# Kernel tuning notes

Measured on AMD Instinct MI355X. Metric: run time of the kernel, lower is better.

## Reference

```python
import jax, jax.numpy as jnp
import numpy as np

B, S, D, H = 4, 2048, 1024, 16
HD = D // H  # head_dim = 64


def setup_inputs() -> dict:
    key = jax.random.key(0)
    ks = jax.random.split(key, 12)
    scale = 1.0 / np.sqrt(D)
    inp = {
        "q": jax.random.normal(ks[0], (B, S, D), jnp.float32),
        "k": jax.random.normal(ks[1], (B, S, D), jnp.float32),
        "v": jax.random.normal(ks[2], (B, S, D), jnp.float32),
        # additive-style mask: 1 = blocked (causal upper triangle)
        "mask": jnp.triu(jnp.ones((S, S), jnp.float32), k=1)[None, None, :, :],
        "Wq": jax.random.normal(ks[3], (D, D), jnp.float32) * scale,
        "bq": jnp.zeros((D,), jnp.float32),
        "Wk": jax.random.normal(ks[4], (D, D), jnp.float32) * scale,
        "bk": jnp.zeros((D,), jnp.float32),
        "Wv": jax.random.normal(ks[5], (D, D), jnp.float32) * scale,
        "bv": jnp.zeros((D,), jnp.float32),
        "Wo": jax.random.normal(ks[6], (D, D), jnp.float32) * scale,
        "bo": jnp.zeros((D,), jnp.float32),
    }
    return inp


def _split_heads(x):
    # [B, S, D] -> [B, H, S, HD]
    b, s, _ = x.shape
    return x.reshape(b, s, H, HD).transpose(0, 2, 1, 3)


def reference(q, k, v, mask, Wq, bq, Wk, bk, Wv, bv, Wo, bo):
    qh = _split_heads(q @ Wq.T + bq)
    kh = _split_heads(k @ Wk.T + bk)
    vh = _split_heads(v @ Wv.T + bv)
    # full [B, H, S, S] score matrix (faithful to the naive implementation)
    logits = jnp.einsum("bhqd,bhkd->bhqk", qh, kh) / jnp.sqrt(jnp.float32(HD))
    logits = logits + mask * -1e9
    weights = jax.nn.softmax(logits, axis=-1)
    attn = jnp.einsum("bhqk,bhkd->bhqd", weights, vh)  # [B, H, S, HD]
    attn = attn.transpose(0, 2, 1, 3).reshape(q.shape[0], -1, D)
    return attn @ Wo.T + bo
```

## Files before the change

### kernel.cpp

```cpp
#include <hip/hip_runtime.h>
#include <stdint.h>

typedef __attribute__((ext_vector_type(8))) short short8;
typedef __attribute__((ext_vector_type(4))) float f32x4;
typedef __attribute__((ext_vector_type(4))) unsigned short ushort4v;
typedef __attribute__((ext_vector_type(8))) unsigned short ushort8v;

#define MFMA(a, b, c) __builtin_amdgcn_mfma_f32_16x16x32_bf16((a), (b), (c), 0, 0, 0)

__device__ __forceinline__ unsigned short f2bf(float f) {
  union { float f; unsigned u; } x; x.f = f;
  return (unsigned short)((x.u + 0x7FFFu + ((x.u >> 16) & 1u)) >> 16);
}

__device__ __forceinline__ unsigned short f2bf_trunc(float f) {
  union { float f; unsigned u; } x; x.f = f;
  return (unsigned short)(x.u >> 16);
}

#define GLL(gp, lp)                                                             \
  __builtin_amdgcn_global_load_lds(                                             \
      (const __attribute__((address_space(1))) unsigned int*)(const void*)(gp), \
      (__attribute__((address_space(3))) unsigned int*)(lp), 16, 0, 0)

__global__ void cvt6_bf16(const float* __restrict__ s0, const float* __restrict__ s1,
                          const float* __restrict__ s2, const float* __restrict__ s3,
                          const float* __restrict__ s4, const float* __restrict__ s5,
                          unsigned short* __restrict__ d0, unsigned short* __restrict__ d1,
                          unsigned short* __restrict__ d2, unsigned short* __restrict__ d3,
                          unsigned short* __restrict__ d4, unsigned short* __restrict__ d5,
                          int nBig, int nSmall) {
  const int y = blockIdx.y;
  const float* s = y == 0 ? s0 : (y == 1 ? s1 : (y == 2 ? s2 :
                   (y == 3 ? s3 : (y == 4 ? s4 : s5))));
  unsigned short* d = y == 0 ? d0 : (y == 1 ? d1 : (y == 2 ? d2 :
                      (y == 3 ? d3 : (y == 4 ? d4 : d5))));
  const int n8 = (y < 3) ? nBig : nSmall;
  int i = blockIdx.x * blockDim.x + threadIdx.x;
  int stride = gridDim.x * blockDim.x;
  for (; i < n8; i += stride) {
    float4 a = ((const float4*)s)[2 * i];
    float4 b = ((const float4*)s)[2 * i + 1];
    ushort8v o;
    o[0] = f2bf(a.x); o[1] = f2bf(a.y); o[2] = f2bf(a.z); o[3] = f2bf(a.w);
    o[4] = f2bf(b.x); o[5] = f2bf(b.y); o[6] = f2bf(b.z); o[7] = f2bf(b.w);
    ((ushort8v*)d)[i] = o;
  }
}

__global__ void cvt_bf16(const float* __restrict__ s, unsigned short* __restrict__ d,
                         int n4) {
  int i = blockIdx.x * blockDim.x + threadIdx.x;
  int stride = gridDim.x * blockDim.x;
  for (; i < n4; i += stride) {
    float4 v = ((const float4*)s)[i];
    ushort4v o;
    o[0] = f2bf(v.x); o[1] = f2bf(v.y); o[2] = f2bf(v.z); o[3] = f2bf(v.w);
    ((ushort4v*)d)[i] = o;
  }
}

template <int OUT_MODE>
__global__ __launch_bounds__(256, 2) void gemm64(
    const unsigned short* __restrict__ A, const unsigned short* __restrict__ W,
    const float* __restrict__ bias, void* __restrict__ Out, float oscale) {
  const int K = 1024, N = 1024;
  __shared__ unsigned short As[2][8192];
  __shared__ unsigned short Bs[2][8192];
  const int tid = threadIdx.x;
  const int lane = tid & 63;
  const int wid = tid >> 6;
  const int l15 = lane & 15, l4 = lane >> 4;
  const int bm = blockIdx.y * 128, bn = blockIdx.x * 128;
  const int wm = (wid >> 1) * 64, wn = (wid & 1) * 64;
  const int srl8 = lane >> 3;
  const int sc8 = ((lane & 7) ^ srl8) * 8;

  f32x4 acc[4][4] = {};

#define STAGE(buf, ktv)                                                        \
  {                                                                            \
    const int kb0 = (ktv) * 64;                                                \
    _Pragma("unroll") for (int i = 0; i < 4; ++i) {                            \
      GLL(&A[(size_t)(bm + i * 32 + wid * 8 + srl8) * K + kb0 + sc8],          \
          &As[buf][i * 2048 + wid * 512]);                                     \
      GLL(&W[(size_t)(bn + i * 32 + wid * 8 + srl8) * K + kb0 + sc8],          \
          &Bs[buf][i * 2048 + wid * 512]);                                     \
    }                                                                          \
  }

  STAGE(0, 0)
  __syncthreads();
  int cur = 0;
  const int NK = K / 64;
  for (int kt = 0; kt < NK; ++kt) {
    if (kt + 1 < NK) STAGE(cur ^ 1, kt + 1)
#pragma unroll
    for (int ks = 0; ks < 2; ++ks) {
      short8 af[4], bfr[4];
#pragma unroll
      for (int i = 0; i < 4; ++i) {
        const int ra = wm + i * 16 + l15;
        const int rb = wn + i * 16 + l15;
        af[i] = *(const short8*)(
            &As[cur][ra * 64 + (((ks * 4 + l4) ^ (ra & 7)) * 8)]);
        bfr[i] = *(const short8*)(
            &Bs[cur][rb * 64 + (((ks * 4 + l4) ^ (rb & 7)) * 8)]);
      }
#pragma unroll
      for (int mi = 0; mi < 4; ++mi)
#pragma unroll
        for (int ni = 0; ni < 4; ++ni)
          acc[mi][ni] = MFMA(af[mi], bfr[ni], acc[mi][ni]);
    }
    __syncthreads();
    cur ^= 1;
  }
#undef STAGE

  float bv[4];
#pragma unroll
  for (int ni = 0; ni < 4; ++ni) bv[ni] = bias[bn + wn + ni * 16 + l15];

#pragma unroll
  for (int mi = 0; mi < 4; ++mi) {
#pragma unroll
    for (int ni = 0; ni < 4; ++ni) {
      const int gn = bn + wn + ni * 16 + l15;
      if constexpr (OUT_MODE == 2) {
        float* Of = (float*)Out;
#pragma unroll
        for (int r = 0; r < 4; ++r) {
          int gm = bm + wm + mi * 16 + l4 * 4 + r;
          Of[(size_t)gm * N + gn] = acc[mi][ni][r] + bv[ni];
        }
      } else {
        unsigned short* Ob = (unsigned short*)Out;
        const int h = gn >> 6, hd = gn & 63;
#pragma unroll
        for (int r = 0; r < 4; ++r) {
          int gm = bm + wm + mi * 16 + l4 * 4 + r;
          int b = gm >> 11, s = gm & 2047;
          Ob[((size_t)(b * 16 + h) * 2048 + s) * 64 + hd] =
              f2bf((acc[mi][ni][r] + bv[ni]) * oscale);
        }
      }
    }
  }
}

__global__ __launch_bounds__(256, 2) void gemm64_kv(
    const unsigned short* __restrict__ A0, const unsigned short* __restrict__ W0,
    const float* __restrict__ bias0, unsigned short* __restrict__ Out0,
    const unsigned short* __restrict__ A1, const unsigned short* __restrict__ W1,
    const float* __restrict__ bias1, unsigned short* __restrict__ Out1) {
  const int K = 1024;
  __shared__ unsigned short As[2][8192];
  __shared__ unsigned short Bs[2][8192];
  const int tid = threadIdx.x;
  const int lane = tid & 63;
  const int wid = tid >> 6;
  const int l15 = lane & 15, l4 = lane >> 4;
  const int proj = blockIdx.y >> 6;
  const int bm = (blockIdx.y & 63) * 128, bn = blockIdx.x * 128;
  const int wm = (wid >> 1) * 64, wn = (wid & 1) * 64;
  const int srl8 = lane >> 3;
  const int sc8 = ((lane & 7) ^ srl8) * 8;

  const unsigned short* A = proj == 0 ? A0 : A1;
  const unsigned short* W = proj == 0 ? W0 : W1;
  const float* bias = proj == 0 ? bias0 : bias1;
  unsigned short* Out = proj == 0 ? Out0 : Out1;

  f32x4 acc[4][4] = {};

#define STAGE(buf, ktv)                                                        \
  {                                                                            \
    const int kb0 = (ktv) * 64;                                                \
    _Pragma("unroll") for (int i = 0; i < 4; ++i) {                            \
      GLL(&A[(size_t)(bm + i * 32 + wid * 8 + srl8) * K + kb0 + sc8],          \
          &As[buf][i * 2048 + wid * 512]);                                     \
      GLL(&W[(size_t)(bn + i * 32 + wid * 8 + srl8) * K + kb0 + sc8],          \
          &Bs[buf][i * 2048 + wid * 512]);                                     \
    }                                                                          \
  }

  STAGE(0, 0)
  __syncthreads();
  int cur = 0;
  const int NK = K / 64;
  for (int kt = 0; kt < NK; ++kt) {
    if (kt + 1 < NK) STAGE(cur ^ 1, kt + 1)
#pragma unroll
    for (int ks = 0; ks < 2; ++ks) {
      short8 af[4], bfr[4];
#pragma unroll
      for (int i = 0; i < 4; ++i) {
        const int ra = wm + i * 16 + l15;
        const int rb = wn + i * 16 + l15;
        af[i] = *(const short8*)(
            &As[cur][ra * 64 + (((ks * 4 + l4) ^ (ra & 7)) * 8)]);
        bfr[i] = *(const short8*)(
            &Bs[cur][rb * 64 + (((ks * 4 + l4) ^ (rb & 7)) * 8)]);
      }
#pragma unroll
      for (int mi = 0; mi < 4; ++mi)
#pragma unroll
        for (int ni = 0; ni < 4; ++ni)
          acc[mi][ni] = MFMA(af[mi], bfr[ni], acc[mi][ni]);
    }
    __syncthreads();
    cur ^= 1;
  }
#undef STAGE

  float bv[4];
#pragma unroll
  for (int ni = 0; ni < 4; ++ni) bv[ni] = bias[bn + wn + ni * 16 + l15];

#pragma unroll
  for (int mi = 0; mi < 4; ++mi) {
#pragma unroll
    for (int ni = 0; ni < 4; ++ni) {
      const int gn = bn + wn + ni * 16 + l15;
      const int h = gn >> 6, hd = gn & 63;
      if (proj == 0) {
#pragma unroll
        for (int r = 0; r < 4; ++r) {
          int gm = bm + wm + mi * 16 + l4 * 4 + r;
          int b = gm >> 11, s = gm & 2047;
          Out[((size_t)(b * 16 + h) * 2048 + s) * 64 + hd] =
              f2bf(acc[mi][ni][r] + bv[ni]);
        }
      } else {
        int gm0 = bm + wm + mi * 16 + l4 * 4;
        int b = gm0 >> 11, s0 = gm0 & 2047;
        ushort4v t;
#pragma unroll
        for (int r = 0; r < 4; ++r) t[r] = f2bf(acc[mi][ni][r] + bv[ni]);
        *(ushort4v*)(Out + ((size_t)(b * 16 + h) * 64 + hd) * 2048 + s0) = t;
      }
    }
  }
}

__global__ __launch_bounds__(256, 3) void attn_kernel(
    const unsigned short* __restrict__ qh, const unsigned short* __restrict__ kh,
    const unsigned short* __restrict__ vt, unsigned short* __restrict__ aout) {
  const int S = 2048, HD = 64;
  __shared__ unsigned short Kt[2][4096];
  __shared__ unsigned short Vt[2][4096];
  __shared__ unsigned short P_lds[4][32 * 72];
  const int tid = threadIdx.x;
  const int wid = tid >> 6, lane = tid & 63;
  const int l15 = lane & 15, l4 = lane >> 4;
  const int bh = blockIdx.x;
  const int b = bh >> 4, h = bh & 15;
  const int yb = 15 - (int)blockIdx.y;
  const int q0 = yb * 128 + wid * 32;
  const unsigned short* Qp = qh + (size_t)bh * S * HD;
  const unsigned short* Kp = kh + (size_t)bh * S * HD;
  const unsigned short* Vp = vt + (size_t)bh * HD * S;
  unsigned short* pl = P_lds[wid];

  const int srl = lane >> 3;
  const int swz = ((lane & 7) ^ srl) * 8;
  const int rb0 = wid * 16, rb1 = wid * 16 + 8;

  short8 vone;
#pragma unroll
  for (int j = 0; j < 8; ++j) vone[j] = (short)0x3F80;

  short8 qa[2][2];
#pragma unroll
  for (int mt = 0; mt < 2; ++mt)
#pragma unroll
    for (int hh = 0; hh < 2; ++hh)
      qa[mt][hh] = *(const short8*)(Qp + (size_t)(q0 + mt * 16 + l15) * HD +
                                    hh * 32 + l4 * 8);

  f32x4 Oacc[2][5] = {};

#define STAGEKV(buf, kbv)                                                      \
  {                                                                            \
    const int k0s = (kbv) << 6;                                                \
    GLL(Kp + (size_t)(k0s + rb0 + srl) * 64 + swz, &Kt[buf][rb0 * 64]);        \
    GLL(Kp + (size_t)(k0s + rb1 + srl) * 64 + swz, &Kt[buf][rb1 * 64]);        \
    GLL(Vp + (size_t)(rb0 + srl) * S + k0s + swz, &Vt[buf][rb0 * 64]);         \
    GLL(Vp + (size_t)(rb1 + srl) * S + k0s + swz, &Vt[buf][rb1 * 64]);         \
  }

  const int nkb = 2 * yb + 2;
  STAGEKV(0, 0)
  __syncthreads();
  int cur = 0;
  for (int kb = 0; kb < nkb; ++kb) {
    const int key0 = kb << 6;
    if (kb + 1 < nkb) STAGEKV(cur ^ 1, kb + 1)

    if (key0 <= q0 + 31) {
      const bool needmask = (key0 + 63 > q0);
      short8 kfr[4][2];
#pragma unroll
      for (int kf = 0; kf < 4; ++kf) {
        const int kr = kf * 16 + l15;
        kfr[kf][0] =
            *(const short8*)(&Kt[cur][kr * 64 + ((l4 ^ (l15 & 7)) * 8)]);
        kfr[kf][1] =
            *(const short8*)(&Kt[cur][kr * 64 + (((4 + l4) ^ (l15 & 7)) * 8)]);
      }
#pragma unroll
      for (int mt = 0; mt < 2; ++mt) {
#pragma unroll
        for (int kf = 0; kf < 4; ++kf) {
          f32x4 z = {};
          z = MFMA(kfr[kf][0], qa[mt][0], z);
          z = MFMA(kfr[kf][1], qa[mt][1], z);
          if (needmask) {
            int qrow = q0 + mt * 16 + l15;
#pragma unroll
            for (int r = 0; r < 4; ++r) {
              int key = key0 + kf * 16 + l4 * 4 + r;
              if (key > qrow) z[r] = -3.0e38f;
            }
          }
          unsigned short* pw = &pl[(mt * 16 + l15) * 72 + kf * 16 + l4 * 4];
#pragma unroll
          for (int r = 0; r < 4; ++r)
            pw[r] = f2bf_trunc(__builtin_amdgcn_exp2f(z[r]));
        }
      }
      short8 vb[4][2];
#pragma unroll
      for (int ni = 0; ni < 4; ++ni) {
        const int vr = ni * 16 + l15;
#pragma unroll
        for (int kc = 0; kc < 2; ++kc)
          vb[ni][kc] = *(const short8*)(
              &Vt[cur][vr * 64 + (((kc * 4 + l4) ^ (l15 & 7)) * 8)]);
      }
      short8 pa[2][2];
#pragma unroll
      for (int mt = 0; mt < 2; ++mt)
#pragma unroll
        for (int kc = 0; kc < 2; ++kc)
          pa[mt][kc] =
              *(const short8*)(&pl[(mt * 16 + l15) * 72 + kc * 32 + l4 * 8]);
#pragma unroll
      for (int mt = 0; mt < 2; ++mt) {
#pragma unroll
        for (int ni = 0; ni < 4; ++ni) {
          Oacc[mt][ni] = MFMA(pa[mt][0], vb[ni][0], Oacc[mt][ni]);
          Oacc[mt][ni] = MFMA(pa[mt][1], vb[ni][1], Oacc[mt][ni]);
        }
        Oacc[mt][4] = MFMA(pa[mt][0], vone, Oacc[mt][4]);
        Oacc[mt][4] = MFMA(pa[mt][1], vone, Oacc[mt][4]);
      }
    }
    __syncthreads();
    cur ^= 1;
  }
#undef STAGEKV

#pragma unroll
  for (int mt = 0; mt < 2; ++mt) {
    float inv[4];
#pragma unroll
    for (int r = 0; r < 4; ++r) inv[r] = __builtin_amdgcn_rcpf(Oacc[mt][4][r]);
#pragma unroll
    for (int ni = 0; ni < 4; ++ni)
#pragma unroll
      for (int r = 0; r < 4; ++r) {
        int row = q0 + mt * 16 + l4 * 4 + r;
        aout[((size_t)(b * 2048 + row)) * 1024 + h * 64 + ni * 16 + l15] =
            f2bf(Oacc[mt][ni][r] * inv[r]);
      }
  }
}

extern "C" void kernel_launch(void* const* d_in, const int* in_sizes, int n_in,
                              void* d_out, int out_size, void* d_ws,
                              size_t ws_size, hipStream_t stream) {
  const float* q = (const float*)d_in[0];
  const float* k = (const float*)d_in[1];
  const float* v = (const float*)d_in[2];
  const float* Wq = (const float*)d_in[4];
  const float* bq = (const float*)d_in[5];
  const float* Wk = (const float*)d_in[6];
  const float* bk = (const float*)d_in[7];
  const float* Wv = (const float*)d_in[8];
  const float* bv = (const float*)d_in[9];
  const float* Wo = (const float*)d_in[10];
  const float* bo = (const float*)d_in[11];

  const size_t MT = (size_t)8192 * 1024;
  unsigned short* qh    = (unsigned short*)d_ws;
  unsigned short* kh    = qh + MT;
  unsigned short* vt    = kh + MT;
  unsigned short* attnb = vt + MT;
  unsigned short* Ab  = (unsigned short*)d_out;
  unsigned short* Wqb = Ab + MT;
  unsigned short* Wkb = Wqb + 1024 * 1024;
  unsigned short* Wvb = Wkb + 1024 * 1024;
  unsigned short* Wob = qh;

  dim3 gg(8, 64), bb(256);
  const int nW4 = 1024 * 1024 / 4;
  const int nW8 = 1024 * 1024 / 8, nA8 = (int)(MT / 8);

  cvt6_bf16<<<dim3(1024, 6), bb, 0, stream>>>(q, k, v, Wq, Wk, Wv,
                                              kh, Ab, attnb, Wqb, Wkb, Wvb,
                                              nA8, nW8);
  gemm64<0><<<gg, bb, 0, stream>>>(kh, Wqb, bq, qh, 0.18033688011112042f);
  gemm64_kv<<<dim3(8, 128), bb, 0, stream>>>(Ab, Wkb, bk, kh, attnb, Wvb, bv, vt);

  attn_kernel<<<dim3(64, 16), bb, 0, stream>>>(qh, kh, vt, attnb);

  cvt_bf16<<<256, bb, 0, stream>>>(Wo, Wob, nW4);
  gemm64<2><<<gg, bb, 0, stream>>>(attnb, Wob, bo, (float*)d_out, 1.0f);
}
```

Measured before the change: 177.2 us.

## Split each attention block's key range across warp pairs and reduce partials in LDS

```diff
diff --git a/kernel.cpp b/kernel.cpp
--- a/kernel.cpp
+++ b/kernel.cpp
@@ -256,8 +256,9 @@
   const int l15 = lane & 15, l4 = lane >> 4;
   const int bh = blockIdx.x;
   const int b = bh >> 4, h = bh & 15;
-  const int yb = 15 - (int)blockIdx.y;
-  const int q0 = yb * 128 + wid * 32;
+  const int qb = 31 - (int)blockIdx.y;
+  const int g = wid >> 1, hf = wid & 1;
+  const int q0 = qb * 64 + g * 32;
   const unsigned short* Qp = qh + (size_t)bh * S * HD;
   const unsigned short* Kp = kh + (size_t)bh * S * HD;
   const unsigned short* Vp = vt + (size_t)bh * HD * S;
@@ -281,33 +282,38 @@
 
   f32x4 Oacc[2][5] = {};
 
-#define STAGEKV(buf, kbv)                                                      \
-  {                                                                            \
-    const int k0s = (kbv) << 6;                                                \
-    GLL(Kp + (size_t)(k0s + rb0 + srl) * 64 + swz, &Kt[buf][rb0 * 64]);        \
-    GLL(Kp + (size_t)(k0s + rb1 + srl) * 64 + swz, &Kt[buf][rb1 * 64]);        \
-    GLL(Vp + (size_t)(rb0 + srl) * S + k0s + swz, &Vt[buf][rb0 * 64]);         \
-    GLL(Vp + (size_t)(rb1 + srl) * S + k0s + swz, &Vt[buf][rb1 * 64]);         \
-  }
-
-  const int nkb = 2 * yb + 2;
-  STAGEKV(0, 0)
-  __syncthreads();
-  int cur = 0;
-  for (int kb = 0; kb < nkb; ++kb) {
-    const int key0 = kb << 6;
-    if (kb + 1 < nkb) STAGEKV(cur ^ 1, kb + 1)
-
-    if (key0 <= q0 + 31) {
-      const bool needmask = (key0 + 63 > q0);
+  const int nt = qb + 1;
+  const int NS = (qb >> 1) + 1;
+  for (int s = 0; s < NS; ++s) {
+    const int tA = 2 * s, tB = 2 * s + 1;
+    {
+      const int k0A = tA << 6;
+      GLL(Kp + (size_t)(k0A + rb0 + srl) * 64 + swz, &Kt[0][rb0 * 64]);
+      GLL(Kp + (size_t)(k0A + rb1 + srl) * 64 + swz, &Kt[0][rb1 * 64]);
+      GLL(Vp + (size_t)(rb0 + srl) * S + k0A + swz, &Vt[0][rb0 * 64]);
+      GLL(Vp + (size_t)(rb1 + srl) * S + k0A + swz, &Vt[0][rb1 * 64]);
+      if (tB < nt) {
+        const int k0B = tB << 6;
+        GLL(Kp + (size_t)(k0B + rb0 + srl) * 64 + swz, &Kt[1][rb0 * 64]);
+        GLL(Kp + (size_t)(k0B + rb1 + srl) * 64 + swz, &Kt[1][rb1 * 64]);
+        GLL(Vp + (size_t)(rb0 + srl) * S + k0B + swz, &Vt[1][rb0 * 64]);
+        GLL(Vp + (size_t)(rb1 + srl) * S + k0B + swz, &Vt[1][rb1 * 64]);
+      }
+    }
+    __syncthreads();
+
+    const int t = 2 * s + hf;
+    if (t < nt) {
+      const int key0 = t << 6;
+      const bool needmask = (t == qb);
       short8 kfr[4][2];
 #pragma unroll
       for (int kf = 0; kf < 4; ++kf) {
         const int kr = kf * 16 + l15;
         kfr[kf][0] =
-            *(const short8*)(&Kt[cur][kr * 64 + ((l4 ^ (l15 & 7)) * 8)]);
+            *(const short8*)(&Kt[hf][kr * 64 + ((l4 ^ (l15 & 7)) * 8)]);
         kfr[kf][1] =
-            *(const short8*)(&Kt[cur][kr * 64 + (((4 + l4) ^ (l15 & 7)) * 8)]);
+            *(const short8*)(&Kt[hf][kr * 64 + (((4 + l4) ^ (l15 & 7)) * 8)]);
       }
 #pragma unroll
       for (int mt = 0; mt < 2; ++mt) {
@@ -337,7 +343,7 @@
 #pragma unroll
         for (int kc = 0; kc < 2; ++kc)
           vb[ni][kc] = *(const short8*)(
-              &Vt[cur][vr * 64 + (((kc * 4 + l4) ^ (l15 & 7)) * 8)]);
+              &Vt[hf][vr * 64 + (((kc * 4 + l4) ^ (l15 & 7)) * 8)]);
       }
       short8 pa[2][2];
 #pragma unroll
@@ -358,23 +364,42 @@
       }
     }
     __syncthreads();
-    cur ^= 1;
-  }
-#undef STAGEKV
-
-#pragma unroll
-  for (int mt = 0; mt < 2; ++mt) {
-    float inv[4];
-#pragma unroll
-    for (int r = 0; r < 4; ++r) inv[r] = __builtin_amdgcn_rcpf(Oacc[mt][4][r]);
-#pragma unroll
-    for (int ni = 0; ni < 4; ++ni)
-#pragma unroll
-      for (int r = 0; r < 4; ++r) {
-        int row = q0 + mt * 16 + l4 * 4 + r;
-        aout[((size_t)(b * 2048 + row)) * 1024 + h * 64 + ni * 16 + l15] =
-            f2bf(Oacc[mt][ni][r] * inv[r]);
-      }
+  }
+
+  if (hf == 1) {
+    f32x4* dst = (f32x4*)((g == 0 ? (float*)&Kt[0][0] : (float*)&Vt[0][0]) +
+                          lane * 40);
+#pragma unroll
+    for (int mt = 0; mt < 2; ++mt)
+#pragma unroll
+      for (int ni = 0; ni < 5; ++ni) dst[mt * 5 + ni] = Oacc[mt][ni];
+  }
+  __syncthreads();
+  if (hf == 0) {
+    const f32x4* src =
+        (const f32x4*)((g == 0 ? (const float*)&Kt[0][0]
+                               : (const float*)&Vt[0][0]) +
+                       lane * 40);
+#pragma unroll
+    for (int mt = 0; mt < 2; ++mt)
+#pragma unroll
+      for (int ni = 0; ni < 5; ++ni) Oacc[mt][ni] += src[mt * 5 + ni];
+
+#pragma unroll
+    for (int mt = 0; mt < 2; ++mt) {
+      float inv[4];
+#pragma unroll
+      for (int r = 0; r < 4; ++r)
+        inv[r] = __builtin_amdgcn_rcpf(Oacc[mt][4][r]);
+#pragma unroll
+      for (int ni = 0; ni < 4; ++ni)
+#pragma unroll
+        for (int r = 0; r < 4; ++r) {
+          int row = q0 + mt * 16 + l4 * 4 + r;
+          aout[((size_t)(b * 2048 + row)) * 1024 + h * 64 + ni * 16 + l15] =
+              f2bf(Oacc[mt][ni][r] * inv[r]);
+        }
+    }
   }
 }
 
@@ -414,7 +439,7 @@
   gemm64<0><<<gg, bb, 0, stream>>>(kh, Wqb, bq, qh, 0.18033688011112042f);
   gemm64_kv<<<dim3(8, 128), bb, 0, stream>>>(Ab, Wkb, bk, kh, attnb, Wvb, bv, vt);
 
-  attn_kernel<<<dim3(64, 16), bb, 0, stream>>>(qh, kh, vt, attnb);
+  attn_kernel<<<dim3(64, 32), bb, 0, stream>>>(qh, kh, vt, attnb);
 
   cvt_bf16<<<256, bb, 0, stream>>>(Wo, Wob, nW4);
   gemm64<2><<<gg, bb, 0, stream>>>(attnb, Wob, bo, (float*)d_out, 1.0f);
```

After: 183.9 us. 3.8% more time.
